# Optimization experiments

Measured on AMD Instinct MI355X. Metric: run time of the kernel, lower is better.

Reference implementation:

```python
import jax, jax.numpy as jnp
import numpy as np

D = 1024
B, T = 4, 2048


def _ln(x, g, b, eps=1e-5):
    mu = jnp.mean(x, axis=-1, keepdims=True)
    var = jnp.mean((x - mu) ** 2, axis=-1, keepdims=True)
    return (x - mu) * jax.lax.rsqrt(var + eps) * g + b


def setup_inputs() -> dict:
    key = jax.random.key(0)
    ks = jax.random.split(key, 24)
    s = 0.02
    lin = lambda k, o, i: jax.random.normal(k, (o, i), jnp.float32) * s
    return {
        "x": jax.random.normal(ks[0], (B, T, D), jnp.float32),
        "g1": jnp.ones((D,), jnp.float32),
        "be1": jnp.zeros((D,), jnp.float32),
        "w_lin1": lin(ks[1], D, D), "b_lin1": jnp.zeros((D,), jnp.float32),
        "wq": lin(ks[2], D, D), "bq": jnp.zeros((D,), jnp.float32),
        "wk": lin(ks[3], D, D), "bk": jnp.zeros((D,), jnp.float32),
        "wv": lin(ks[4], D, D), "bv": jnp.zeros((D,), jnp.float32),
        "w_lin2": lin(ks[5], D, D), "b_lin2": jnp.zeros((D,), jnp.float32),
        "g2": jnp.ones((D,), jnp.float32),
        "be2": jnp.zeros((D,), jnp.float32),
        "w_ff1": lin(ks[6], 2 * D, D), "b_ff1": jnp.zeros((2 * D,), jnp.float32),
        "w_ff2": lin(ks[7], D, 2 * D), "b_ff2": jnp.zeros((D,), jnp.float32),
    }


def reference(x, g1, be1, w_lin1, b_lin1, wq, bq, wk, bk, wv, bv,
              w_lin2, b_lin2, g2, be2, w_ff1, b_ff1, w_ff2, b_ff2):
    # x: [B,T,D]. Torch Linear: y = x @ W.T + b with W: [out,in]
    x = _ln(x, g1, be1)
    x = x @ w_lin1.T + b_lin1
    # single-head self-attention, scale = 1/sqrt(d_model) (matches source)
    q = x @ wq.T + bq
    k = x @ wk.T + bk
    v = x @ wv.T + bv
    scores = jnp.einsum('btd,bsd->bts', q, k) / jnp.sqrt(jnp.float32(x.shape[-1]))
    mask = jnp.tril(jnp.ones((x.shape[1], x.shape[1]), bool))  # [T,T]
    scores = jnp.where(mask, scores, -jnp.inf)
    probs = jax.nn.softmax(scores, axis=-1)
    attn = jnp.einsum('bts,bsd->btd', probs, v)
    x = x + (attn @ w_lin2.T + b_lin2)
    # FFN on norm2(x), exact (erf) GELU as torch default
    h = _ln(x, g2, be2)
    h = jax.nn.gelu(h @ w_ff1.T + b_ff1, approximate=False)
    x = x + (h @ w_ff2.T + b_ff2)
    return x
```

## Files before the change

### kernel.cpp

```cpp
#include <hip/hip_runtime.h>

typedef __attribute__((ext_vector_type(4))) float f32x4;
typedef __attribute__((ext_vector_type(8))) short short8;
typedef __attribute__((ext_vector_type(4))) unsigned short u16x4;
typedef __attribute__((ext_vector_type(8))) unsigned short u16x8;

#define MFMA(a, b, c) __builtin_amdgcn_mfma_f32_16x16x32_bf16(a, b, c, 0, 0, 0)
#define GLOAD16(g, l) __builtin_amdgcn_global_load_lds( \
    (const __attribute__((address_space(1))) unsigned int*)(g), \
    (__attribute__((address_space(3))) unsigned int*)(l), 16, 0, 0)

__device__ inline unsigned short f2bf(float f) {
    unsigned int u = __float_as_uint(f);
    u += 0x7fffu + ((u >> 16) & 1u);
    return (unsigned short)(u >> 16);
}

__global__ __launch_bounds__(256) void cvt_kernel(const float* __restrict__ in,
                                                  unsigned short* __restrict__ out, int n4,
                                                  float scale) {
    int i = blockIdx.x * 256 + threadIdx.x;
    if (i < n4) {
        f32x4 v = *(const f32x4*)(in + (long long)i * 4);
        u16x4 o;
#pragma unroll
        for (int j = 0; j < 4; j++) o[j] = f2bf(v[j] * scale);
        *(u16x4*)&out[(long long)i * 4] = o;
    }
}

__global__ __launch_bounds__(256) void biascat_kernel(const float* __restrict__ bq,
                                                      const float* __restrict__ bk,
                                                      float* __restrict__ out) {
    int i = blockIdx.x * 256 + threadIdx.x;
    if (i < 1024) out[i] = bq[i] * 0.03125f;
    else if (i < 2048) out[i] = bk[i - 1024];
}

__global__ __launch_bounds__(256) void ln_kernel(const float* __restrict__ x,
                                                 const float* __restrict__ g,
                                                 const float* __restrict__ be,
                                                 unsigned short* __restrict__ out) {
    const int row = blockIdx.x, tid = threadIdx.x;
    const float* px = x + (long long)row * 1024;
    f32x4 v = *(const f32x4*)(px + tid * 4);
    float s = v[0] + v[1] + v[2] + v[3];
    float q = v[0] * v[0] + v[1] * v[1] + v[2] * v[2] + v[3] * v[3];
#pragma unroll
    for (int o = 32; o; o >>= 1) { s += __shfl_xor(s, o); q += __shfl_xor(q, o); }
    __shared__ float sm[10];
    const int lane = tid & 63, wid = tid >> 6;
    if (lane == 0) { sm[wid] = s; sm[4 + wid] = q; }
    __syncthreads();
    if (tid == 0) {
        float ts = sm[0] + sm[1] + sm[2] + sm[3];
        float tq = sm[4] + sm[5] + sm[6] + sm[7];
        float mean = ts * (1.f / 1024.f);
        float var = tq * (1.f / 1024.f) - mean * mean;
        sm[8] = mean; sm[9] = rsqrtf(var + 1e-5f);
    }
    __syncthreads();
    float mean = sm[8], rs = sm[9];
    f32x4 gg = *(const f32x4*)(g + tid * 4);
    f32x4 bb = *(const f32x4*)(be + tid * 4);
    u16x4 o;
#pragma unroll
    for (int i = 0; i < 4; i++) o[i] = f2bf((v[i] - mean) * rs * gg[i] + bb[i]);
    *(u16x4*)&out[(long long)row * 1024 + tid * 4] = o;
}

__global__ __launch_bounds__(256) void softmax_kernel(float* __restrict__ S) {
    const int T = 2048;
    const int t = blockIdx.x, b = blockIdx.y, tid = threadIdx.x;
    float* row = S + ((long long)b * T + t) * T;
    const int base = tid * 8;
    f32x4 v0 = *(const f32x4*)(row + base);
    f32x4 v1 = *(const f32x4*)(row + base + 4);
    float mx = -1e30f;
#pragma unroll
    for (int i = 0; i < 4; i++) {
        if (base + i <= t)     mx = fmaxf(mx, v0[i]);
        if (base + 4 + i <= t) mx = fmaxf(mx, v1[i]);
    }
#pragma unroll
    for (int o = 32; o; o >>= 1) mx = fmaxf(mx, __shfl_xor(mx, o));
    __shared__ float sm[10];
    const int lane = tid & 63, wid = tid >> 6;
    if (lane == 0) sm[wid] = mx;
    __syncthreads();
    if (tid == 0) sm[8] = fmaxf(fmaxf(sm[0], sm[1]), fmaxf(sm[2], sm[3]));
    __syncthreads();
    float M = sm[8];
    float e[8]; float s = 0.f;
#pragma unroll
    for (int i = 0; i < 4; i++) {
        e[i]     = (base + i <= t)     ? __expf(v0[i] - M) : 0.f;
        e[4 + i] = (base + 4 + i <= t) ? __expf(v1[i] - M) : 0.f;
        s += e[i] + e[4 + i];
    }
#pragma unroll
    for (int o = 32; o; o >>= 1) s += __shfl_xor(s, o);
    if (lane == 0) sm[4 + wid] = s;
    __syncthreads();
    if (tid == 0) sm[9] = 1.f / (sm[4] + sm[5] + sm[6] + sm[7]);
    __syncthreads();
    float inv = sm[9];
    unsigned short* P = (unsigned short*)row;
    u16x8 o;
#pragma unroll
    for (int i = 0; i < 8; i++) o[i] = f2bf(e[i] * inv);
    *(u16x8*)&P[base] = o;
}

template <int MODE>
__global__ __launch_bounds__(256) void gemm128(
    const unsigned short* __restrict__ A, int lda, long long sA,
    const unsigned short* __restrict__ Bw, int ldb, long long sB,
    const float* __restrict__ bias,
    const float* __restrict__ resid, long long sR,
    float* __restrict__ outf, unsigned short* __restrict__ outb,
    int ldo, long long sO, int K, float scale, int flags) {
    const int m0 = blockIdx.y * 128, n0 = blockIdx.x * 128;
    if ((flags & 1) && n0 > m0) return;
    const int bz = blockIdx.z;
    A += (long long)bz * sA; Bw += (long long)bz * sB;
    if (resid) resid += (long long)bz * sR;
    if (outf) outf += (long long)bz * sO;
    if (outb) outb += (long long)bz * sO;
    const int Keff = (flags & 2) ? (m0 + 128 < K ? m0 + 128 : K) : K;

    __shared__ __align__(16) unsigned short LDS[2 * 8192];
    unsigned short* As = LDS;
    unsigned short* Bs = LDS + 8192;

    const int tid = threadIdx.x, lane = tid & 63, wid = tid >> 6;

    const unsigned short* srcA[4]; const unsigned short* srcB[4]; int dst[4];
#pragma unroll
    for (int l = 0; l < 4; l++) {
        int p = l * 256 + tid;
        int r = p >> 3, cs = (p & 7) ^ (r & 7);
        srcA[l] = A + (long long)(m0 + r) * lda + cs * 8;
        srcB[l] = Bw + (long long)(n0 + r) * ldb + cs * 8;
        dst[l] = l * 2048 + wid * 512;
    }

    const int wm = (wid >> 1) * 64, wn = (wid & 1) * 64;
    const int fr = lane & 15, kq = lane >> 4;
    int ao[4][2], bo[4][2];
#pragma unroll
    for (int i = 0; i < 4; i++) {
        int ra = wm + i * 16 + fr, rb = wn + i * 16 + fr;
#pragma unroll
        for (int s = 0; s < 2; s++) {
            ao[i][s] = ra * 64 + (((s * 4 + kq) ^ (ra & 7)) * 8);
            bo[i][s] = rb * 64 + (((s * 4 + kq) ^ (rb & 7)) * 8);
        }
    }

    f32x4 acc[4][4] = {};
    for (int k0 = 0; k0 < Keff; k0 += 64) {
#pragma unroll
        for (int l = 0; l < 4; l++) GLOAD16(srcA[l] + k0, As + dst[l]);
#pragma unroll
        for (int l = 0; l < 4; l++) GLOAD16(srcB[l] + k0, Bs + dst[l]);
        __syncthreads();
        {
            short8 a[4], b[4];
#pragma unroll
            for (int i = 0; i < 4; i++) { a[i] = *(const short8*)&As[ao[i][0]];
                                          b[i] = *(const short8*)&Bs[bo[i][0]]; }
#pragma unroll
            for (int i = 0; i < 4; i++)
#pragma unroll
                for (int j = 0; j < 4; j++)
                    acc[i][j] = MFMA(a[i], b[j], acc[i][j]);
#pragma unroll
            for (int i = 0; i < 4; i++) { a[i] = *(const short8*)&As[ao[i][1]];
                                          b[i] = *(const short8*)&Bs[bo[i][1]]; }
#pragma unroll
            for (int i = 0; i < 4; i++)
#pragma unroll
                for (int j = 0; j < 4; j++)
                    acc[i][j] = MFMA(a[i], b[j], acc[i][j]);
        }
        __syncthreads();
    }

    const int cc = lane & 15, rr = (lane >> 4) * 4;
#pragma unroll
    for (int fm = 0; fm < 4; fm++)
#pragma unroll
        for (int fn = 0; fn < 4; fn++) {
            f32x4 av = acc[fm][fn];
            int colg = n0 + wn + fn * 16 + cc;
            int rowg0 = m0 + wm + fm * 16 + rr;
            float bv = bias ? bias[colg] : 0.f;
            if (MODE == 3) {
                u16x4 o;
#pragma unroll
                for (int i = 0; i < 4; i++) o[i] = f2bf((av[i] + bv) * scale);
                *(u16x4*)&outb[(long long)colg * ldo + rowg0] = o;
            } else {
#pragma unroll
                for (int i = 0; i < 4; i++) {
                    float v = av[i] + bv;
                    long long idx = (long long)(rowg0 + i) * ldo + colg;
                    if (MODE == 0) outf[idx] = v;
                    if (MODE == 1) outf[idx] = v + resid[idx];
                    if (MODE == 2) outb[idx] = f2bf(v * scale);
                    if (MODE == 4) { outf[idx] = v; outb[idx] = f2bf(v); }
                    if (MODE == 5) outb[idx] = f2bf(0.5f * v * (1.f + erff(v * 0.70710678f)));
                }
            }
        }
}

extern "C" void kernel_launch(void* const* d_in, const int* in_sizes, int n_in,
                              void* d_out, int out_size, void* d_ws, size_t ws_size,
                              hipStream_t stream) {
    const float* x      = (const float*)d_in[0];
    const float* g1     = (const float*)d_in[1];
    const float* be1    = (const float*)d_in[2];
    const float* b_lin1 = (const float*)d_in[4];
    const float* bq     = (const float*)d_in[6];
    const float* bk     = (const float*)d_in[8];
    const float* bv     = (const float*)d_in[10];
    const float* b_lin2 = (const float*)d_in[12];
    const float* g2     = (const float*)d_in[13];
    const float* be2    = (const float*)d_in[14];
    const float* b_ff1  = (const float*)d_in[16];
    const float* b_ff2  = (const float*)d_in[18];

    const long long MB = 1024LL * 1024LL;
    char* ws = (char*)d_ws;
    unsigned short* xn1 = (unsigned short*)(ws + 0);
    unsigned short* x1b = (unsigned short*)(ws + 16 * MB);
    float*          S   = (float*)(ws + 0);
    float*          bqk = (float*)(ws + 60 * MB);
    float*          x1f = (float*)(ws + 64 * MB);
    unsigned short* xn2 = (unsigned short*)(ws + 64 * MB);
    unsigned short* qk  = (unsigned short*)(ws + 96 * MB);
    unsigned short* vT  = (unsigned short*)(ws + 128 * MB);
    unsigned short* attn= (unsigned short*)(ws + 96 * MB);
    unsigned short* h   = (unsigned short*)(ws + 96 * MB);
    float*          x2  = (float*)(ws + 144 * MB);
    unsigned short* wb1 = (unsigned short*)(ws + 176 * MB);
    unsigned short* wbq = (unsigned short*)(ws + 178 * MB);
    unsigned short* wbk = (unsigned short*)(ws + 180 * MB);
    unsigned short* wbv = (unsigned short*)(ws + 182 * MB);
    unsigned short* wb2 = (unsigned short*)(ws + 184 * MB);
    unsigned short* wbf1= (unsigned short*)(ws + 186 * MB);
    unsigned short* wbf2= (unsigned short*)(ws + 190 * MB);

    auto cvt = [&](const void* src, unsigned short* dst, long long n, float sc) {
        int n4 = (int)(n / 4);
        cvt_kernel<<<(n4 + 255) / 256, 256, 0, stream>>>((const float*)src, dst, n4, sc);
    };
    cvt(d_in[3], wb1, 1048576, 1.f);
    cvt(d_in[5], wbq, 1048576, 0.03125f);
    cvt(d_in[7], wbk, 1048576, 1.f);
    cvt(d_in[9], wbv, 1048576, 1.f);
    cvt(d_in[11], wb2, 1048576, 1.f);
    cvt(d_in[15], wbf1, 2097152, 1.f);
    cvt(d_in[17], wbf2, 2097152, 1.f);
    biascat_kernel<<<8, 256, 0, stream>>>(bq, bk, bqk);

    ln_kernel<<<8192, 256, 0, stream>>>(x, g1, be1, xn1);
    gemm128<4><<<dim3(8, 64, 1), 256, 0, stream>>>(xn1, 1024, 0, wb1, 1024, 0, b_lin1,
        nullptr, 0, x1f, x1b, 1024, 0, 1024, 1.f, 0);
    gemm128<2><<<dim3(16, 64, 1), 256, 0, stream>>>(x1b, 1024, 0, wbq, 1024, 0, bqk,
        nullptr, 0, nullptr, qk, 2048, 0, 1024, 1.f, 0);
    gemm128<3><<<dim3(8, 16, 4), 256, 0, stream>>>(x1b, 1024, 2048LL * 1024, wbv, 1024, 0, bv,
        nullptr, 0, nullptr, vT, 2048, 2097152LL, 1024, 1.f, 0);
    gemm128<0><<<dim3(16, 16, 4), 256, 0, stream>>>(qk, 2048, 4194304LL, qk + 1024, 2048, 4194304LL,
        nullptr, nullptr, 0, S, nullptr, 2048, 4194304LL, 1024, 1.f, 1);
    softmax_kernel<<<dim3(2048, 4), 256, 0, stream>>>(S);
    gemm128<2><<<dim3(8, 16, 4), 256, 0, stream>>>((unsigned short*)S, 4096, 8388608LL,
        vT, 2048, 2097152LL, nullptr, nullptr, 0, nullptr, attn, 1024, 2097152LL, 2048, 1.f, 2);
    gemm128<1><<<dim3(8, 64, 1), 256, 0, stream>>>(attn, 1024, 0, wb2, 1024, 0, b_lin2,
        x1f, 0, x2, nullptr, 1024, 0, 1024, 1.f, 0);
    ln_kernel<<<8192, 256, 0, stream>>>(x2, g2, be2, xn2);
    gemm128<5><<<dim3(16, 64, 1), 256, 0, stream>>>(xn2, 1024, 0, wbf1, 1024, 0, b_ff1,
        nullptr, 0, nullptr, h, 2048, 0, 1024, 1.f, 0);
    gemm128<1><<<dim3(8, 64, 1), 256, 0, stream>>>(h, 2048, 0, wbf2, 2048, 0, b_ff2,
        x2, 0, (float*)d_out, nullptr, 1024, 0, 2048, 1.f, 0);
}
```

Before: 545.1 us.

## Double-buffer LDS tiles in gemm128 to overlap global loads with MFMA

Doubles the GEMM kernel's shared-memory buffer and prefetches the next K tile into the alternate buffer while MFMAs run on the current one. Each iteration now ends with a single vmcnt wait and barrier instead of two syncthreads around a serialized load-then-compute step. The launch bound is also raised to ask for two blocks per CU. This hides global-to-LDS latency behind compute, at the cost of 64KB of LDS per block, which may limit occupancy and make the two-block request hard to meet.

Result: faster. 483.2 us (-11.4%).

```diff
diff --git a/kernel.cpp b/kernel.cpp
--- a/kernel.cpp
+++ b/kernel.cpp
@@ -9,6 +9,8 @@
 #define GLOAD16(g, l) __builtin_amdgcn_global_load_lds( \
     (const __attribute__((address_space(1))) unsigned int*)(g), \
     (__attribute__((address_space(3))) unsigned int*)(l), 16, 0, 0)
+#define BARX() __builtin_amdgcn_s_barrier()
+#define VM0 asm volatile("s_waitcnt vmcnt(0)" ::: "memory")
 
 __device__ inline unsigned short f2bf(float f) {
     unsigned int u = __float_as_uint(f);
@@ -113,7 +115,7 @@
 }
 
 template <int MODE>
-__global__ __launch_bounds__(256) void gemm128(
+__global__ __launch_bounds__(256, 2) void gemm128(
     const unsigned short* __restrict__ A, int lda, long long sA,
     const unsigned short* __restrict__ Bw, int ldb, long long sB,
     const float* __restrict__ bias,
@@ -128,10 +130,9 @@
     if (outf) outf += (long long)bz * sO;
     if (outb) outb += (long long)bz * sO;
     const int Keff = (flags & 2) ? (m0 + 128 < K ? m0 + 128 : K) : K;
-
-    __shared__ __align__(16) unsigned short LDS[2 * 8192];
-    unsigned short* As = LDS;
-    unsigned short* Bs = LDS + 8192;
+    const int nt = Keff >> 6;
+
+    __shared__ __align__(16) unsigned short LDS[2 * 16384];
 
     const int tid = threadIdx.x, lane = tid & 63, wid = tid >> 6;
 
@@ -154,37 +155,49 @@
 #pragma unroll
         for (int s = 0; s < 2; s++) {
             ao[i][s] = ra * 64 + (((s * 4 + kq) ^ (ra & 7)) * 8);
-            bo[i][s] = rb * 64 + (((s * 4 + kq) ^ (rb & 7)) * 8);
+            bo[i][s] = 8192 + rb * 64 + (((s * 4 + kq) ^ (rb & 7)) * 8);
         }
     }
 
     f32x4 acc[4][4] = {};
-    for (int k0 = 0; k0 < Keff; k0 += 64) {
-#pragma unroll
-        for (int l = 0; l < 4; l++) GLOAD16(srcA[l] + k0, As + dst[l]);
-#pragma unroll
-        for (int l = 0; l < 4; l++) GLOAD16(srcB[l] + k0, Bs + dst[l]);
-        __syncthreads();
-        {
-            short8 a[4], b[4];
-#pragma unroll
-            for (int i = 0; i < 4; i++) { a[i] = *(const short8*)&As[ao[i][0]];
-                                          b[i] = *(const short8*)&Bs[bo[i][0]]; }
-#pragma unroll
-            for (int i = 0; i < 4; i++)
-#pragma unroll
-                for (int j = 0; j < 4; j++)
-                    acc[i][j] = MFMA(a[i], b[j], acc[i][j]);
-#pragma unroll
-            for (int i = 0; i < 4; i++) { a[i] = *(const short8*)&As[ao[i][1]];
-                                          b[i] = *(const short8*)&Bs[bo[i][1]]; }
-#pragma unroll
-            for (int i = 0; i < 4; i++)
-#pragma unroll
-                for (int j = 0; j < 4; j++)
-                    acc[i][j] = MFMA(a[i], b[j], acc[i][j]);
+
+#pragma unroll
+    for (int l = 0; l < 4; l++) GLOAD16(srcA[l], LDS + dst[l]);
+#pragma unroll
+    for (int l = 0; l < 4; l++) GLOAD16(srcB[l], LDS + 8192 + dst[l]);
+    VM0; BARX();
+
+    int c = 0;
+    for (int t = 0; t < nt; ++t) {
+        if (t + 1 < nt) {
+            const int kn = (t + 1) * 64;
+            unsigned short* Lp = LDS + (c ^ 1) * 16384;
+#pragma unroll
+            for (int l = 0; l < 4; l++) GLOAD16(srcA[l] + kn, Lp + dst[l]);
+#pragma unroll
+            for (int l = 0; l < 4; l++) GLOAD16(srcB[l] + kn, Lp + 8192 + dst[l]);
         }
-        __syncthreads();
+        const unsigned short* Lc = LDS + c * 16384;
+        short8 a[4], b[4];
+#pragma unroll
+        for (int i = 0; i < 4; i++) { a[i] = *(const short8*)&Lc[ao[i][0]];
+                                      b[i] = *(const short8*)&Lc[bo[i][0]]; }
+#pragma unroll
+        for (int i = 0; i < 4; i++)
+#pragma unroll
+            for (int j = 0; j < 4; j++)
+                acc[i][j] = MFMA(a[i], b[j], acc[i][j]);
+#pragma unroll
+        for (int i = 0; i < 4; i++) { a[i] = *(const short8*)&Lc[ao[i][1]];
+                                      b[i] = *(const short8*)&Lc[bo[i][1]]; }
+#pragma unroll
+        for (int i = 0; i < 4; i++)
+#pragma unroll
+            for (int j = 0; j < 4; j++)
+                acc[i][j] = MFMA(a[i], b[j], acc[i][j]);
+        VM0;
+        BARX();
+        c ^= 1;
     }
 
     const int cc = lane & 15, rr = (lane >> 4) * 4;
```
